# Optimization experiments

Measured on AMD Instinct MI355X. Metric: run time of the kernel, lower is better.

The kernel has to match this reference:

```python
import jax, jax.numpy as jnp
import numpy as np

HEAD_SIZE = 128
EMB_SIZE = 2048


def setup_inputs() -> dict:
    key = jax.random.key(0)
    kx, kq, kk, kv = jax.random.split(key, 4)
    B, T, C = 4, 4096, EMB_SIZE
    scale = 1.0 / np.sqrt(C)
    x = jax.random.normal(kx, (B, T, C), dtype=jnp.float32)
    # Linear(emb, head, bias=False) weights stored as [emb, head] for x @ W
    Wq = jax.random.normal(kq, (C, HEAD_SIZE), dtype=jnp.float32) * scale
    Wk = jax.random.normal(kk, (C, HEAD_SIZE), dtype=jnp.float32) * scale
    Wv = jax.random.normal(kv, (C, HEAD_SIZE), dtype=jnp.float32) * scale
    return {"x": x, "Wq": Wq, "Wk": Wk, "Wv": Wv}


def reference(x, Wq, Wk, Wv):
    B, T, C = x.shape
    q = jnp.einsum("btc,ch->bth", x, Wq)
    k = jnp.einsum("btc,ch->bth", x, Wk)
    v = jnp.einsum("btc,ch->bth", x, Wv)
    # NOTE: original code scales by C ** (-0.05), where C = emb_size
    scale = jnp.asarray(C, dtype=x.dtype) ** (-0.05)
    wei = jnp.einsum("bqh,bkh->bqk", q, k) * scale  # [B, T, T]
    causal = jnp.tril(jnp.ones((T, T), dtype=bool))
    wei = jnp.where(causal[None, :, :], wei, -jnp.inf)
    wei = jax.nn.softmax(wei, axis=-1)
    # dropout(p=0.2) treated as identity (eval mode) for a deterministic reference
    out = jnp.einsum("bqk,bkh->bqh", wei, v)  # [B, T, head]
    return out
```

## Files before the change

kernel.cpp:

```cpp
#include <hip/hip_runtime.h>

#define LOG2E 1.4426950408889634f
#define SCALE 0.6830207f

typedef __attribute__((ext_vector_type(8))) _Float16 f16x8;
typedef __attribute__((ext_vector_type(4))) _Float16 f16x4;
typedef __attribute__((ext_vector_type(4))) float f32x4;

__device__ __forceinline__ void wg_barrier() {
  asm volatile("s_waitcnt lgkmcnt(0)\n\ts_barrier" ::: "memory");
}

__global__ __launch_bounds__(256) void prep_wf(const float* __restrict__ Wq,
    const float* __restrict__ Wk, const float* __restrict__ Wv,
    _Float16* __restrict__ Wf) {
  int t = blockIdx.x * 256 + threadIdx.x;
  int lane = t & 63;
  int nt = (t >> 6) % 24;
  int kc = t / (64 * 24);
  int g = lane >> 4, c = lane & 15;
  int n = nt * 16 + c;
  const float* W = (n < 128) ? Wq : ((n < 256) ? Wk : Wv);
  int nn = n & 127;
  f16x8 o;
#pragma unroll
  for (int j = 0; j < 8; ++j) {
    int k = kc * 32 + g * 8 + j;
    o[j] = (_Float16)W[k * 128 + nn];
  }
  *(f16x8*)(Wf + (size_t)t * 8) = o;
}

__global__ __launch_bounds__(256, 2) void proj(const float* __restrict__ x,
    const _Float16* __restrict__ Wf,
    _Float16* __restrict__ qo, _Float16* __restrict__ ko,
    _Float16* __restrict__ vTo) {
  __shared__ __align__(16) _Float16 As[2][32 * 72];
  int tid = threadIdx.x;
  int wave = tid >> 6, lane = tid & 63;
  int g = lane >> 4, c = lane & 15;
  int m0 = blockIdx.x * 32;
  int wn = wave * 6;
  const f32x4 fz = {0.f, 0.f, 0.f, 0.f};
  f32x4 acc[2][6];
#pragma unroll
  for (int a = 0; a < 2; ++a)
#pragma unroll
    for (int q = 0; q < 6; ++q) acc[a][q] = fz;

  int r = tid >> 3, c4 = tid & 7;
  const float* xp = x + (size_t)(m0 + r) * 2048 + c4 * 8;
  float4 pa[4], pb[4];
#pragma unroll
  for (int z = 0; z < 4; ++z) {
    pa[z] = *(const float4*)(xp + z * 64);
    pb[z] = *(const float4*)(xp + z * 64 + 4);
  }
  {
    f16x8 h8;
    h8[0] = (_Float16)pa[0].x; h8[1] = (_Float16)pa[0].y;
    h8[2] = (_Float16)pa[0].z; h8[3] = (_Float16)pa[0].w;
    h8[4] = (_Float16)pb[0].x; h8[5] = (_Float16)pb[0].y;
    h8[6] = (_Float16)pb[0].z; h8[7] = (_Float16)pb[0].w;
    *(f16x8*)(&As[0][0] + r * 72 + c4 * 8) = h8;
  }
  wg_barrier();

#pragma unroll 4
  for (int kb = 0; kb < 32; ++kb) {
    if (kb + 1 < 32) {
      int s = (kb + 1) & 3;
      f16x8 h8;
      h8[0] = (_Float16)pa[s].x; h8[1] = (_Float16)pa[s].y;
      h8[2] = (_Float16)pa[s].z; h8[3] = (_Float16)pa[s].w;
      h8[4] = (_Float16)pb[s].x; h8[5] = (_Float16)pb[s].y;
      h8[6] = (_Float16)pb[s].z; h8[7] = (_Float16)pb[s].w;
      *(f16x8*)(&As[(kb + 1) & 1][0] + r * 72 + c4 * 8) = h8;
    }
    if (kb + 4 < 32) {
      pa[kb & 3] = *(const float4*)(xp + (kb + 4) * 64);
      pb[kb & 3] = *(const float4*)(xp + (kb + 4) * 64 + 4);
    }
    const _Float16* Ab = &As[kb & 1][0];
#pragma unroll
    for (int kcl = 0; kcl < 2; ++kcl) {
      f16x8 af[2];
#pragma unroll
      for (int mt = 0; mt < 2; ++mt)
        af[mt] = *(const f16x8*)(Ab + (mt * 16 + c) * 72 + kcl * 32 + g * 8);
#pragma unroll
      for (int nt = 0; nt < 6; ++nt) {
        size_t boff = ((size_t)((kb * 2 + kcl) * 24 + wn + nt) * 64 + lane) * 8;
        f16x8 bf = *(const f16x8*)(Wf + boff);
#pragma unroll
        for (int mt = 0; mt < 2; ++mt)
          acc[mt][nt] = __builtin_amdgcn_mfma_f32_16x16x32_f16(af[mt], bf, acc[mt][nt], 0, 0, 0);
      }
    }
    wg_barrier();
  }
#pragma unroll
  for (int mt = 0; mt < 2; ++mt) {
#pragma unroll
    for (int nt = 0; nt < 6; ++nt) {
      int n = (wn + nt) * 16 + c;
      int mat = n >> 7, col = n & 127;
#pragma unroll
      for (int i = 0; i < 4; ++i) {
        int row = m0 + mt * 16 + g * 4 + i;
        _Float16 hv = (_Float16)acc[mt][nt][i];
        if (mat == 0)      qo[(size_t)row * 128 + col] = hv;
        else if (mat == 1) ko[(size_t)row * 128 + col] = hv;
        else               vTo[(size_t)col * 16384 + row] = hv;
      }
    }
  }
}

__global__ __launch_bounds__(256, 3) void attn_part(
    const _Float16* __restrict__ qg, const _Float16* __restrict__ kg,
    const _Float16* __restrict__ vT,
    float* __restrict__ Op, float* __restrict__ Ml) {
  __shared__ __align__(16) _Float16 Ks[64 * 136];
  __shared__ __align__(16) _Float16 Vt[128 * 72];
  __shared__ __align__(16) _Float16 Ps[4][16 * 72];
  int tid = threadIdx.x;
  int wave = tid >> 6, lane = tid & 63;
  int g = lane >> 4, c = lane & 15;
  int u = blockIdx.x;
  int b = u / 160, t = u % 160;
  int qt, ch;
  if (t < 16)      { qt = t;                 ch = 0; }
  else if (t < 48) { qt = 16 + (t - 16) / 2; ch = (t - 16) % 2; }
  else if (t < 96) { qt = 32 + (t - 48) / 3; ch = (t - 48) % 3; }
  else             { qt = 48 + (t - 96) / 4; ch = (t - 96) % 4; }
  int q0 = qt * 64;
  int jbeg = ch * 16, jend = min(jbeg + 16, qt + 1);
  size_t base = (size_t)b * 4096 * 128;

  f16x8 qf[4];
#pragma unroll
  for (int kc = 0; kc < 4; ++kc)
    qf[kc] = *(const f16x8*)(qg + base + (size_t)(q0 + wave * 16 + c) * 128 + kc * 32 + g * 8);

  const f32x4 fz = {0.f, 0.f, 0.f, 0.f};
  f32x4 o[8];
#pragma unroll
  for (int hh = 0; hh < 8; ++hh) o[hh] = fz;
  float mrow = -1e30f, lrow = 0.f;

  int kr = tid >> 4, kc8 = tid & 15;
  int vh = tid >> 3, vt8 = tid & 7;
  uint4 rk[4], rv[4];
#pragma unroll
  for (int z = 0; z < 4; ++z) {
    rk[z] = *(const uint4*)(kg + base + (size_t)(jbeg * 64 + z * 16 + kr) * 128 + kc8 * 8);
    rv[z] = *(const uint4*)(vT + (size_t)(z * 32 + vh) * 16384 + b * 4096 + jbeg * 64 + vt8 * 8);
  }

  for (int j = jbeg; j < jend; ++j) {
    wg_barrier();
#pragma unroll
    for (int z = 0; z < 4; ++z) {
      *(uint4*)(Ks + (z * 16 + kr) * 136 + kc8 * 8) = rk[z];
      *(uint4*)(Vt + (z * 32 + vh) * 72 + vt8 * 8) = rv[z];
    }
    if (j + 1 < jend) {
#pragma unroll
      for (int z = 0; z < 4; ++z) {
        rk[z] = *(const uint4*)(kg + base + (size_t)((j + 1) * 64 + z * 16 + kr) * 128 + kc8 * 8);
        rv[z] = *(const uint4*)(vT + (size_t)(z * 32 + vh) * 16384 + b * 4096 + (j + 1) * 64 + vt8 * 8);
      }
    }
    wg_barrier();

    f32x4 s[4];
#pragma unroll
    for (int mt = 0; mt < 4; ++mt) s[mt] = fz;
#pragma unroll
    for (int kc = 0; kc < 4; ++kc) {
#pragma unroll
      for (int mt = 0; mt < 4; ++mt) {
        f16x8 kf = *(const f16x8*)(Ks + (mt * 16 + c) * 136 + kc * 32 + g * 8);
        s[mt] = __builtin_amdgcn_mfma_f32_16x16x32_f16(kf, qf[kc], s[mt], 0, 0, 0);
      }
    }
    bool diag = (j == qt);
    float tmax = -1e30f;
#pragma unroll
    for (int mt = 0; mt < 4; ++mt)
#pragma unroll
      for (int i = 0; i < 4; ++i) {
        float v = s[mt][i] * SCALE;
        if (diag && (mt * 16 + g * 4 + i) > (wave * 16 + c)) v = -1e30f;
        s[mt][i] = v;
        tmax = fmaxf(tmax, v);
      }
    tmax = fmaxf(tmax, __shfl_xor(tmax, 16, 64));
    tmax = fmaxf(tmax, __shfl_xor(tmax, 32, 64));
    float mnew = fmaxf(mrow, tmax);
    float alpha = __builtin_amdgcn_exp2f((mrow - mnew) * LOG2E);
    float p[4][4];
    float rsum = 0.f;
#pragma unroll
    for (int mt = 0; mt < 4; ++mt)
#pragma unroll
      for (int i = 0; i < 4; ++i) {
        float e = __builtin_amdgcn_exp2f((s[mt][i] - mnew) * LOG2E);
        p[mt][i] = e;
        rsum += e;
      }
    rsum += __shfl_xor(rsum, 16, 64);
    rsum += __shfl_xor(rsum, 32, 64);
    lrow = lrow * alpha + rsum;
    mrow = mnew;
    int srcb = (lane & 48) + ((lane & 48) >> 2);
    float ar[4];
#pragma unroll
    for (int i = 0; i < 4; ++i) ar[i] = __shfl(alpha, srcb + i, 64);
#pragma unroll
    for (int hh = 0; hh < 8; ++hh)
#pragma unroll
      for (int i = 0; i < 4; ++i) o[hh][i] *= ar[i];
#pragma unroll
    for (int mt = 0; mt < 4; ++mt) {
      f16x4 pk;
#pragma unroll
      for (int i = 0; i < 4; ++i) pk[i] = (_Float16)p[mt][i];
      *(f16x4*)(&Ps[wave][0] + c * 72 + mt * 16 + g * 4) = pk;
    }
#pragma unroll
    for (int kc = 0; kc < 2; ++kc) {
      f16x8 pf = *(const f16x8*)(&Ps[wave][0] + c * 72 + kc * 32 + g * 8);
#pragma unroll
      for (int hh = 0; hh < 8; ++hh) {
        f16x8 vf = *(const f16x8*)(Vt + (hh * 16 + c) * 72 + kc * 32 + g * 8);
        o[hh] = __builtin_amdgcn_mfma_f32_16x16x32_f16(pf, vf, o[hh], 0, 0, 0);
      }
    }
  }
#pragma unroll
  for (int hh = 0; hh < 8; ++hh)
#pragma unroll
    for (int i = 0; i < 4; ++i) {
      int row = wave * 16 + g * 4 + i;
      Op[(size_t)u * 8192 + row * 128 + hh * 16 + c] = o[hh][i];
    }
  if (lane < 16) {
    int row = wave * 16 + lane;
    Ml[(size_t)u * 128 + row * 2]     = mrow;
    Ml[(size_t)u * 128 + row * 2 + 1] = lrow;
  }
}

__global__ __launch_bounds__(256) void attn_merge(const float* __restrict__ Op,
    const float* __restrict__ Ml, float* __restrict__ out) {
  int bq = blockIdx.x;
  int b = bq >> 6, qt = bq & 63;
  int nch = qt / 16 + 1;
  int bb = (qt < 16) ? qt : (qt < 32) ? 16 + 2 * (qt - 16)
           : (qt < 48) ? 48 + 3 * (qt - 32) : 96 + 4 * (qt - 48);
  int u0 = b * 160 + bb;
  __shared__ float w[4][64];
  int tid = threadIdx.x;
  if (tid < 64) {
    float m[4], l[4];
    float M = -1e30f;
    for (int uu = 0; uu < nch; ++uu) {
      m[uu] = Ml[(size_t)(u0 + uu) * 128 + tid * 2];
      l[uu] = Ml[(size_t)(u0 + uu) * 128 + tid * 2 + 1];
      M = fmaxf(M, m[uu]);
    }
    float L = 0.f;
    for (int uu = 0; uu < nch; ++uu) {
      float e = __builtin_amdgcn_exp2f((m[uu] - M) * LOG2E);
      w[uu][tid] = e;
      L += l[uu] * e;
    }
    float iL = 1.0f / L;
    for (int uu = 0; uu < nch; ++uu) w[uu][tid] *= iL;
  }
  __syncthreads();
  for (int it = 0; it < 32; ++it) {
    int idx = it * 256 + tid;
    int row = idx >> 7;
    float acc = 0.f;
    for (int uu = 0; uu < nch; ++uu)
      acc += w[uu][row] * Op[(size_t)(u0 + uu) * 8192 + idx];
    out[(size_t)b * 4096 * 128 + (size_t)qt * 8192 + idx] = acc;
  }
}

extern "C" void kernel_launch(void* const* d_in, const int* in_sizes, int n_in,
                              void* d_out, int out_size, void* d_ws, size_t ws_size,
                              hipStream_t stream) {
  const float* x  = (const float*)d_in[0];
  const float* Wq = (const float*)d_in[1];
  const float* Wk = (const float*)d_in[2];
  const float* Wv = (const float*)d_in[3];
  const size_t NTOK = (size_t)16384 * 128;
  _Float16* q  = (_Float16*)d_ws;
  _Float16* k  = q + NTOK;
  _Float16* vT = k + NTOK;
  _Float16* Wf = vT + NTOK;
  float* Op = (float*)(Wf + (size_t)786432);
  float* Ml = Op + (size_t)640 * 8192;
  prep_wf<<<384, 256, 0, stream>>>(Wq, Wk, Wv, Wf);
  proj<<<512, 256, 0, stream>>>(x, Wf, q, k, vT);
  attn_part<<<640, 256, 0, stream>>>(q, k, vT, Op, Ml);
  attn_merge<<<256, 256, 0, stream>>>(Op, Ml, (float*)d_out);
}
```

Baseline: 399.3 us.

## Read K/V fragments directly from global memory and remap blocks per XCD

Removes the LDS staging of K and V tiles, along with its register prefetch and both workgroup barriers per iteration. Each wave now loads its MFMA K and V^T fragments straight from global memory and relies on L2 and the cache for reuse across waves. Block IDs are remapped so each XCD handles half of a single batch, which keeps that batch's K/V working set local to one L2. Launch bounds rise to 4 blocks per CU. In exchange, every wave issues redundant global loads with no software prefetch, so latency is exposed inside the inner loop.

```diff
diff --git a/kernel.cpp b/kernel.cpp
--- a/kernel.cpp
+++ b/kernel.cpp
@@ -117,18 +117,19 @@
   }
 }
 
-__global__ __launch_bounds__(256, 3) void attn_part(
+__global__ __launch_bounds__(256, 4) void attn_part(
     const _Float16* __restrict__ qg, const _Float16* __restrict__ kg,
     const _Float16* __restrict__ vT,
     float* __restrict__ Op, float* __restrict__ Ml) {
-  __shared__ __align__(16) _Float16 Ks[64 * 136];
-  __shared__ __align__(16) _Float16 Vt[128 * 72];
   __shared__ __align__(16) _Float16 Ps[4][16 * 72];
   int tid = threadIdx.x;
   int wave = tid >> 6, lane = tid & 63;
   int g = lane >> 4, c = lane & 15;
-  int u = blockIdx.x;
-  int b = u / 160, t = u % 160;
+  int up = blockIdx.x;
+  int xcd = up & 7, slot = up >> 3;
+  int b = xcd >> 1;
+  int t = (xcd & 1) * 80 + slot;
+  int u = b * 160 + t;
   int qt, ch;
   if (t < 16)      { qt = t;                 ch = 0; }
   else if (t < 48) { qt = 16 + (t - 16) / 2; ch = (t - 16) % 2; }
@@ -137,6 +138,8 @@
   int q0 = qt * 64;
   int jbeg = ch * 16, jend = min(jbeg + 16, qt + 1);
   size_t base = (size_t)b * 4096 * 128;
+  const _Float16* kb_ = kg + base;
+  const _Float16* vb_ = vT + (size_t)b * 4096;
 
   f16x8 qf[4];
 #pragma unroll
@@ -149,31 +152,7 @@
   for (int hh = 0; hh < 8; ++hh) o[hh] = fz;
   float mrow = -1e30f, lrow = 0.f;
 
-  int kr = tid >> 4, kc8 = tid & 15;
-  int vh = tid >> 3, vt8 = tid & 7;
-  uint4 rk[4], rv[4];
-#pragma unroll
-  for (int z = 0; z < 4; ++z) {
-    rk[z] = *(const uint4*)(kg + base + (size_t)(jbeg * 64 + z * 16 + kr) * 128 + kc8 * 8);
-    rv[z] = *(const uint4*)(vT + (size_t)(z * 32 + vh) * 16384 + b * 4096 + jbeg * 64 + vt8 * 8);
-  }
-
   for (int j = jbeg; j < jend; ++j) {
-    wg_barrier();
-#pragma unroll
-    for (int z = 0; z < 4; ++z) {
-      *(uint4*)(Ks + (z * 16 + kr) * 136 + kc8 * 8) = rk[z];
-      *(uint4*)(Vt + (z * 32 + vh) * 72 + vt8 * 8) = rv[z];
-    }
-    if (j + 1 < jend) {
-#pragma unroll
-      for (int z = 0; z < 4; ++z) {
-        rk[z] = *(const uint4*)(kg + base + (size_t)((j + 1) * 64 + z * 16 + kr) * 128 + kc8 * 8);
-        rv[z] = *(const uint4*)(vT + (size_t)(z * 32 + vh) * 16384 + b * 4096 + (j + 1) * 64 + vt8 * 8);
-      }
-    }
-    wg_barrier();
-
     f32x4 s[4];
 #pragma unroll
     for (int mt = 0; mt < 4; ++mt) s[mt] = fz;
@@ -181,7 +160,7 @@
     for (int kc = 0; kc < 4; ++kc) {
 #pragma unroll
       for (int mt = 0; mt < 4; ++mt) {
-        f16x8 kf = *(const f16x8*)(Ks + (mt * 16 + c) * 136 + kc * 32 + g * 8);
+        f16x8 kf = *(const f16x8*)(kb_ + (size_t)(j * 64 + mt * 16 + c) * 128 + kc * 32 + g * 8);
         s[mt] = __builtin_amdgcn_mfma_f32_16x16x32_f16(kf, qf[kc], s[mt], 0, 0, 0);
       }
     }
@@ -200,14 +179,13 @@
     tmax = fmaxf(tmax, __shfl_xor(tmax, 32, 64));
     float mnew = fmaxf(mrow, tmax);
     float alpha = __builtin_amdgcn_exp2f((mrow - mnew) * LOG2E);
-    float p[4][4];
     float rsum = 0.f;
 #pragma unroll
     for (int mt = 0; mt < 4; ++mt)
 #pragma unroll
       for (int i = 0; i < 4; ++i) {
         float e = __builtin_amdgcn_exp2f((s[mt][i] - mnew) * LOG2E);
-        p[mt][i] = e;
+        s[mt][i] = e;
         rsum += e;
       }
     rsum += __shfl_xor(rsum, 16, 64);
@@ -226,7 +204,7 @@
     for (int mt = 0; mt < 4; ++mt) {
       f16x4 pk;
 #pragma unroll
-      for (int i = 0; i < 4; ++i) pk[i] = (_Float16)p[mt][i];
+      for (int i = 0; i < 4; ++i) pk[i] = (_Float16)s[mt][i];
       *(f16x4*)(&Ps[wave][0] + c * 72 + mt * 16 + g * 4) = pk;
     }
 #pragma unroll
@@ -234,7 +212,7 @@
       f16x8 pf = *(const f16x8*)(&Ps[wave][0] + c * 72 + kc * 32 + g * 8);
 #pragma unroll
       for (int hh = 0; hh < 8; ++hh) {
-        f16x8 vf = *(const f16x8*)(Vt + (hh * 16 + c) * 72 + kc * 32 + g * 8);
+        f16x8 vf = *(const f16x8*)(vb_ + (size_t)(hh * 16 + c) * 16384 + j * 64 + kc * 32 + g * 8);
         o[hh] = __builtin_amdgcn_mfma_f32_16x16x32_f16(pf, vf, o[hh], 0, 0, 0);
       }
     }
```

Result: slower. 450.9 us (+12.9%).
